# Kernel optimization log

Hardware: AMD Instinct MI355X
Metric: run time of the kernel (lower is better)

## Reference

```python
import jax, jax.numpy as jnp
import numpy as np

B, L, HID = 4, 512, 512
H, DH = 8, 64  # num_attention_heads, attention_head_size (== rel embed size)


def setup_inputs() -> dict:
    key = jax.random.key(0)
    ks = jax.random.split(key, 9)
    s = 1.0 / np.sqrt(HID)
    return {
        "hidden_states": jax.random.normal(ks[0], (B, L, HID), jnp.float32),
        "heads": jnp.zeros((B, 1, L, L), jnp.float32),  # additive mask, 0 = valid arc
        "rels": jax.random.normal(ks[1], (B, L, L, DH), jnp.float32),
        "Wq": jax.random.normal(ks[2], (HID, HID), jnp.float32) * s,
        "bq": jnp.zeros((HID,), jnp.float32),
        "Wk": jax.random.normal(ks[3], (HID, HID), jnp.float32) * s,
        "bk": jnp.zeros((HID,), jnp.float32),
        "Wv": jax.random.normal(ks[4], (HID, HID), jnp.float32) * s,
        "bv": jnp.zeros((HID,), jnp.float32),
    }


def _heads_split(x):
    # (B, L, H*DH) -> (B, H, L, DH)
    return x.reshape(B, L, H, DH).transpose(0, 2, 1, 3)


def reference(hidden_states, heads, rels, Wq, bq, Wk, bk, Wv, bv):
    q = _heads_split(hidden_states @ Wq.T + bq)  # (B,H,L,DH)
    k = _heads_split(hidden_states @ Wk.T + bk)
    v = _heads_split(hidden_states @ Wv.T + bv)

    scores = jnp.einsum("bhqd,bhkd->bhqk", q, k)
    # relation-augmented scores: sum_d q[b,h,q,d] * rels[b,q,k,d]
    rel_scores = jnp.einsum("bhqd,bqkd->bhqk", q, rels)
    scores = (scores + rel_scores) / np.sqrt(DH) + heads  # heads broadcasts over H

    probs = jax.nn.softmax(scores, axis=-1)  # dropout is identity at eval

    ctx = jnp.einsum("bhqk,bhkd->bhqd", probs, v)
    # relation-weighted values: sum_k probs[b,h,q,k] * rels[b,q,k,d]
    ctx = ctx + jnp.einsum("bhqk,bqkd->bhqd", probs, rels)

    return ctx.transpose(0, 2, 1, 3).reshape(B, L, H * DH)
```

## Files before the change

### kernel.cpp

```cpp
#include <hip/hip_runtime.h>
#include <stdint.h>


__global__ __launch_bounds__(256)
void wtrans(const float* __restrict__ Wq, const float* __restrict__ Wk,
            const float* __restrict__ Wv, float* __restrict__ WT)
{
    __shared__ float tile[64*65];
    const int z  = blockIdx.z;
    const float* W = (z==0) ? Wq : (z==1) ? Wk : Wv;
    const int kt = blockIdx.x * 64;
    const int ot = blockIdx.y * 64;
    const int t  = threadIdx.x;

    {
        const int c4 = (t & 15) * 4;
        #pragma unroll
        for (int i = 0; i < 4; i++) {
            const int r = (t >> 4) + i*16;
            const float4 v4 = *(const float4*)(W + (size_t)(ot + r)*512 + kt + c4);
            tile[r*65 + c4 + 0] = v4.x;
            tile[r*65 + c4 + 1] = v4.y;
            tile[r*65 + c4 + 2] = v4.z;
            tile[r*65 + c4 + 3] = v4.w;
        }
    }
    __syncthreads();
    {
        const int c4 = (t & 15) * 4;
        float* dst = WT + (size_t)z*262144;
        #pragma unroll
        for (int i = 0; i < 4; i++) {
            const int r2 = (t >> 4) + i*16;
            float4 v4;
            v4.x = tile[(c4+0)*65 + r2];
            v4.y = tile[(c4+1)*65 + r2];
            v4.z = tile[(c4+2)*65 + r2];
            v4.w = tile[(c4+3)*65 + r2];
            *(float4*)(dst + (size_t)(kt + r2)*512 + ot + c4) = v4;
        }
    }
}

__global__ __launch_bounds__(256)
void qkv_gemm(const float* __restrict__ X, const float* __restrict__ WT,
              const float* __restrict__ bq, const float* __restrict__ bk,
              const float* __restrict__ bv,
              float* __restrict__ qf, float* __restrict__ kTb, float* __restrict__ vf)
{
    __shared__ __align__(16) float Xs[16][512];
    const int z  = blockIdx.y;
    const int m0 = blockIdx.x * 16;
    const float* WTz = WT + (size_t)z*262144;
    const float* bb  = (z==0) ? bq : (z==1) ? bk : bv;

    const int t = threadIdx.x;
    {
        const int r = t >> 4, c0 = (t & 15) * 32;
        const float4* src = (const float4*)(X + (size_t)(m0 + r)*512 + c0);
        float4* dstl = (float4*)(&Xs[r][c0]);
        #pragma unroll
        for (int i = 0; i < 8; i++) dstl[i] = src[i];
    }
    __syncthreads();

    const int ob   = t & 127;
    const int msub = (t >> 7) * 8;
    float acc[8][4] = {};

    #pragma unroll 2
    for (int k = 0; k < 512; k += 4) {
        float w[4][4];
        #pragma unroll
        for (int kk = 0; kk < 4; kk++)
            #pragma unroll
            for (int j = 0; j < 4; j++)
                w[kk][j] = WTz[(size_t)(k+kk)*512 + ob + 128*j];
        #pragma unroll
        for (int mm = 0; mm < 8; mm++) {
            const float4 x4 = *(const float4*)(&Xs[msub + mm][k]);
            #pragma unroll
            for (int j = 0; j < 4; j++) {
                acc[mm][j] = fmaf(x4.x, w[0][j], acc[mm][j]);
                acc[mm][j] = fmaf(x4.y, w[1][j], acc[mm][j]);
                acc[mm][j] = fmaf(x4.z, w[2][j], acc[mm][j]);
                acc[mm][j] = fmaf(x4.w, w[3][j], acc[mm][j]);
            }
        }
    }

    const int b     = m0 >> 9;
    const int lbase = (m0 & 511) + msub;
    #pragma unroll
    for (int j = 0; j < 4; j++) {
        const int o = ob + 128*j;
        const float bo = bb[o];
        const int h = o >> 6, d = o & 63;
        if (z == 1) {
            float* dst = kTb + ((size_t)(b*8 + h)*64 + d)*512 + lbase;
            *(float4*)(dst + 0) = make_float4(acc[0][j]+bo, acc[1][j]+bo,
                                              acc[2][j]+bo, acc[3][j]+bo);
            *(float4*)(dst + 4) = make_float4(acc[4][j]+bo, acc[5][j]+bo,
                                              acc[6][j]+bo, acc[7][j]+bo);
        } else {
            float* dst = ((z==0) ? qf : vf) + ((size_t)(b*8 + h)*512 + lbase)*64 + d;
            #pragma unroll
            for (int mm = 0; mm < 8; mm++) dst[(size_t)mm*64] = acc[mm][j] + bo;
        }
    }
}

__global__ __launch_bounds__(512)
void attn_flash(const float* __restrict__ qf, const float* __restrict__ kT,
                const float* __restrict__ vf, const float* __restrict__ rels,
                const float* __restrict__ heads, float* __restrict__ out)
{
    __shared__ __align__(16) float rl[4*64*64];

    const int bid = blockIdx.x;
    const int wg  = (bid & 7) * 64 + (bid >> 3);
    const int b   = wg >> 7;
    const int q0  = (wg & 127) * 4;

    const int t = threadIdx.x, h = t >> 6, lane = t & 63;

    const float* kTh = kT + ((size_t)(b*8 + h)*64)*512;
    const float* vfh = vf + ((size_t)(b*8 + h)*512)*64;
    const float* qh  = qf + ((size_t)(b*8 + h)*512 + q0)*64;

    float ctx[4] = {0.f, 0.f, 0.f, 0.f};
    float m[4]   = {-3.0e38f, -3.0e38f, -3.0e38f, -3.0e38f};
    float s[4]   = {0.f, 0.f, 0.f, 0.f};

    const int sqi = t >> 7;
    const int su  = t & 127;
    const int sk  = su >> 1;
    const int sdh = (su & 1) * 32;
    const int sc4 = sdh >> 2;
    const int skx = sk & 15;
    const float* srcq = rels + ((size_t)(b*512 + q0 + sqi))*512*64;
    float* wb = rl + sqi*4096 + sk*64;

    for (int kt = 0; kt < 8; kt++) {
        __syncthreads();
        {
            const float* src = srcq + ((size_t)(kt*64 + sk))*64 + sdh;
            #pragma unroll
            for (int i = 0; i < 8; i++) {
                const float4 v4 = *(const float4*)(src + 4*i);
                *(float4*)(wb + 4*((sc4 + i) ^ skx)) = v4;
            }
        }
        __syncthreads();

        const int kg = kt*64 + lane;
        const int kx4 = lane & 15;
        const float* rr = rl + lane*64;
        float sc[4] = {0.f, 0.f, 0.f, 0.f};
        #pragma unroll 4
        for (int d0 = 0; d0 < 64; d0 += 4) {
            const float k0 = kTh[(size_t)(d0+0)*512 + kg];
            const float k1 = kTh[(size_t)(d0+1)*512 + kg];
            const float k2 = kTh[(size_t)(d0+2)*512 + kg];
            const float k3 = kTh[(size_t)(d0+3)*512 + kg];
            #pragma unroll
            for (int qi = 0; qi < 4; qi++) {
                const float4 q4 = *(const float4*)(qh + (size_t)qi*64 + d0);
                const float4 r4 = *(const float4*)(rr + qi*4096
                                                   + 4*((d0 >> 2) ^ kx4));
                float a = sc[qi];
                a = fmaf(q4.x, k0, a);  a = fmaf(q4.x, r4.x, a);
                a = fmaf(q4.y, k1, a);  a = fmaf(q4.y, r4.y, a);
                a = fmaf(q4.z, k2, a);  a = fmaf(q4.z, r4.z, a);
                a = fmaf(q4.w, k3, a);  a = fmaf(q4.w, r4.w, a);
                sc[qi] = a;
            }
        }

        float P[4];
        #pragma unroll
        for (int qi = 0; qi < 4; qi++) {
            float S = sc[qi]*0.125f
                    + heads[((size_t)(b*512 + q0 + qi))*512 + kg];
            float mt = S;
            #pragma unroll
            for (int w = 1; w < 64; w <<= 1) mt = fmaxf(mt, __shfl_xor(mt, w));
            const float mn = fmaxf(m[qi], mt);
            const float al = __expf(m[qi] - mn);
            const float p  = __expf(S - mn);
            float ps = p;
            #pragma unroll
            for (int w = 1; w < 64; w <<= 1) ps += __shfl_xor(ps, w);
            s[qi]   = s[qi]*al + ps;
            ctx[qi] = ctx[qi]*al;
            m[qi]   = mn;
            P[qi]   = p;
        }

        const float* vtile = vfh + (size_t)(kt*64)*64 + lane;
        const int l3 = lane & 3, lc = lane >> 2;
        #pragma unroll 8
        for (int kk = 0; kk < 64; kk++) {
            const float v = vtile[(size_t)kk*64];
            const float* rb = rl + kk*64 + (l3 | ((lc ^ (kk & 15)) << 2));
            #pragma unroll
            for (int qi = 0; qi < 4; qi++) {
                const float pk = __int_as_float(
                    __builtin_amdgcn_readlane(__float_as_int(P[qi]), kk));
                ctx[qi] = fmaf(pk, v + rb[qi*4096], ctx[qi]);
            }
        }
    }

    #pragma unroll
    for (int qi = 0; qi < 4; qi++)
        out[((size_t)(b*512 + q0 + qi))*512 + h*64 + lane] = ctx[qi] / s[qi];
}

extern "C" void kernel_launch(void* const* d_in, const int* in_sizes, int n_in,
                              void* d_out, int out_size, void* d_ws, size_t ws_size,
                              hipStream_t stream)
{
    (void)in_sizes; (void)n_in; (void)out_size; (void)ws_size;

    const float* hidden = (const float*)d_in[0];
    const float* heads  = (const float*)d_in[1];
    const float* rels   = (const float*)d_in[2];
    const float* Wq = (const float*)d_in[3];
    const float* bq = (const float*)d_in[4];
    const float* Wk = (const float*)d_in[5];
    const float* bk = (const float*)d_in[6];
    const float* Wv = (const float*)d_in[7];
    const float* bv = (const float*)d_in[8];
    float* outF = (float*)d_out;

    float* ws = (float*)d_ws;
    float* qf  = ws;
    float* kTb = ws + 1048576;
    float* vf  = ws + 2097152;

    float* WT = outF;

    wtrans<<<dim3(8, 8, 3), 256, 0, stream>>>(Wq, Wk, Wv, WT);
    qkv_gemm<<<dim3(128, 3), 256, 0, stream>>>(hidden, WT, bq, bk, bv, qf, kTb, vf);
    attn_flash<<<dim3(512), 512, 0, stream>>>(qf, kTb, vf, rels, heads, outF);
}
```

Before: 581.1 us.

## Register-prefetch rels tiles, vectorize PV loop and retile QKV GEMM

The attention kernel now loads the next rels tile into registers while computing on the current tile held in shared memory, so global latency overlaps compute. The P·(V+R) loop is remapped so each lane owns one query and four head dims, using float4 loads of V and rels instead of scalar loads per query. The QKV GEMM uses 8-row tiles with float4 weight loads and float4 output stores, and launches twice as many blocks. The trade-off is more register pressure from the staging buffer, plus select logic to pick per-lane softmax values.

```diff
diff --git a/kernel.cpp b/kernel.cpp
--- a/kernel.cpp
+++ b/kernel.cpp
@@ -48,64 +48,62 @@
               const float* __restrict__ bv,
               float* __restrict__ qf, float* __restrict__ kTb, float* __restrict__ vf)
 {
-    __shared__ __align__(16) float Xs[16][512];
+    __shared__ __align__(16) float Xs[8][512];
     const int z  = blockIdx.y;
-    const int m0 = blockIdx.x * 16;
+    const int m0 = blockIdx.x * 8;
     const float* WTz = WT + (size_t)z*262144;
     const float* bb  = (z==0) ? bq : (z==1) ? bk : bv;
 
     const int t = threadIdx.x;
     {
-        const int r = t >> 4, c0 = (t & 15) * 32;
+        const int r = t >> 5, c0 = (t & 31) * 16;
         const float4* src = (const float4*)(X + (size_t)(m0 + r)*512 + c0);
-        float4* dstl = (float4*)(&Xs[r][c0]);
-        #pragma unroll
-        for (int i = 0; i < 8; i++) dstl[i] = src[i];
+        float4* d4 = (float4*)(&Xs[r][c0]);
+        d4[0]=src[0]; d4[1]=src[1]; d4[2]=src[2]; d4[3]=src[3];
     }
     __syncthreads();
 
-    const int ob   = t & 127;
-    const int msub = (t >> 7) * 8;
-    float acc[8][4] = {};
+    const int o0 = (t & 127) * 4;
+    const int mh = (t >> 7) * 4;
+    float acc[4][4] = {};
 
     #pragma unroll 2
     for (int k = 0; k < 512; k += 4) {
-        float w[4][4];
+        float4 w4[4];
         #pragma unroll
         for (int kk = 0; kk < 4; kk++)
-            #pragma unroll
-            for (int j = 0; j < 4; j++)
-                w[kk][j] = WTz[(size_t)(k+kk)*512 + ob + 128*j];
-        #pragma unroll
-        for (int mm = 0; mm < 8; mm++) {
-            const float4 x4 = *(const float4*)(&Xs[msub + mm][k]);
+            w4[kk] = *(const float4*)(WTz + (size_t)(k+kk)*512 + o0);
+        #pragma unroll
+        for (int mm = 0; mm < 4; mm++) {
+            const float4 x4 = *(const float4*)(&Xs[mh + mm][k]);
             #pragma unroll
             for (int j = 0; j < 4; j++) {
-                acc[mm][j] = fmaf(x4.x, w[0][j], acc[mm][j]);
-                acc[mm][j] = fmaf(x4.y, w[1][j], acc[mm][j]);
-                acc[mm][j] = fmaf(x4.z, w[2][j], acc[mm][j]);
-                acc[mm][j] = fmaf(x4.w, w[3][j], acc[mm][j]);
+                acc[mm][j] = fmaf(x4.x, ((const float*)&w4[0])[j], acc[mm][j]);
+                acc[mm][j] = fmaf(x4.y, ((const float*)&w4[1])[j], acc[mm][j]);
+                acc[mm][j] = fmaf(x4.z, ((const float*)&w4[2])[j], acc[mm][j]);
+                acc[mm][j] = fmaf(x4.w, ((const float*)&w4[3])[j], acc[mm][j]);
             }
         }
     }
 
-    const int b     = m0 >> 9;
-    const int lbase = (m0 & 511) + msub;
-    #pragma unroll
-    for (int j = 0; j < 4; j++) {
-        const int o = ob + 128*j;
-        const float bo = bb[o];
-        const int h = o >> 6, d = o & 63;
-        if (z == 1) {
-            float* dst = kTb + ((size_t)(b*8 + h)*64 + d)*512 + lbase;
-            *(float4*)(dst + 0) = make_float4(acc[0][j]+bo, acc[1][j]+bo,
-                                              acc[2][j]+bo, acc[3][j]+bo);
-            *(float4*)(dst + 4) = make_float4(acc[4][j]+bo, acc[5][j]+bo,
-                                              acc[6][j]+bo, acc[7][j]+bo);
-        } else {
-            float* dst = ((z==0) ? qf : vf) + ((size_t)(b*8 + h)*512 + lbase)*64 + d;
-            #pragma unroll
-            for (int mm = 0; mm < 8; mm++) dst[(size_t)mm*64] = acc[mm][j] + bo;
+    const float4 b4 = *(const float4*)(bb + o0);
+    const int b = m0 >> 9, lbase = (m0 & 511) + mh;
+    const int h = o0 >> 6, d0 = o0 & 63;
+    if (z == 1) {
+        #pragma unroll
+        for (int j = 0; j < 4; j++) {
+            const float bj = ((const float*)&b4)[j];
+            const float4 vv = make_float4(acc[0][j]+bj, acc[1][j]+bj,
+                                          acc[2][j]+bj, acc[3][j]+bj);
+            *(float4*)(kTb + ((size_t)(b*8 + h)*64 + d0 + j)*512 + lbase) = vv;
+        }
+    } else {
+        float* dst = (z==0) ? qf : vf;
+        #pragma unroll
+        for (int mm = 0; mm < 4; mm++) {
+            const float4 vv = make_float4(acc[mm][0]+b4.x, acc[mm][1]+b4.y,
+                                          acc[mm][2]+b4.z, acc[mm][3]+b4.w);
+            *(float4*)(dst + ((size_t)(b*8 + h)*512 + lbase + mm)*64 + d0) = vv;
         }
     }
 }
@@ -128,7 +126,11 @@
     const float* vfh = vf + ((size_t)(b*8 + h)*512)*64;
     const float* qh  = qf + ((size_t)(b*8 + h)*512 + q0)*64;
 
-    float ctx[4] = {0.f, 0.f, 0.f, 0.f};
+    const int qp = lane >> 4;
+    const int dq = lane & 15;
+    const float* vq = vfh + 4*dq;
+
+    float ctx4[4] = {0.f, 0.f, 0.f, 0.f};
     float m[4]   = {-3.0e38f, -3.0e38f, -3.0e38f, -3.0e38f};
     float s[4]   = {0.f, 0.f, 0.f, 0.f};
 
@@ -138,20 +140,25 @@
     const int sdh = (su & 1) * 32;
     const int sc4 = sdh >> 2;
     const int skx = sk & 15;
-    const float* srcq = rels + ((size_t)(b*512 + q0 + sqi))*512*64;
+    const float* srcq = rels + ((size_t)(b*512 + q0 + sqi))*512*64
+                             + (size_t)sk*64 + sdh;
     float* wb = rl + sqi*4096 + sk*64;
+
+    float4 stg[8];
+    #pragma unroll
+    for (int i = 0; i < 8; i++) stg[i] = *(const float4*)(srcq + 4*i);
 
     for (int kt = 0; kt < 8; kt++) {
         __syncthreads();
-        {
-            const float* src = srcq + ((size_t)(kt*64 + sk))*64 + sdh;
-            #pragma unroll
-            for (int i = 0; i < 8; i++) {
-                const float4 v4 = *(const float4*)(src + 4*i);
-                *(float4*)(wb + 4*((sc4 + i) ^ skx)) = v4;
-            }
-        }
+        #pragma unroll
+        for (int i = 0; i < 8; i++)
+            *(float4*)(wb + 4*((sc4 + i) ^ skx)) = stg[i];
         __syncthreads();
+        if (kt < 7) {
+            const float* nsrc = srcq + (size_t)(kt+1)*64*64;
+            #pragma unroll
+            for (int i = 0; i < 8; i++) stg[i] = *(const float4*)(nsrc + 4*i);
+        }
 
         const int kg = kt*64 + lane;
         const int kx4 = lane & 15;
@@ -177,7 +184,7 @@
             }
         }
 
-        float P[4];
+        float P[4], al[4];
         #pragma unroll
         for (int qi = 0; qi < 4; qi++) {
             float S = sc[qi]*0.125f
@@ -186,35 +193,45 @@
             #pragma unroll
             for (int w = 1; w < 64; w <<= 1) mt = fmaxf(mt, __shfl_xor(mt, w));
             const float mn = fmaxf(m[qi], mt);
-            const float al = __expf(m[qi] - mn);
+            al[qi] = __expf(m[qi] - mn);
             const float p  = __expf(S - mn);
             float ps = p;
             #pragma unroll
             for (int w = 1; w < 64; w <<= 1) ps += __shfl_xor(ps, w);
-            s[qi]   = s[qi]*al + ps;
-            ctx[qi] = ctx[qi]*al;
-            m[qi]   = mn;
-            P[qi]   = p;
-        }
-
-        const float* vtile = vfh + (size_t)(kt*64)*64 + lane;
-        const int l3 = lane & 3, lc = lane >> 2;
+            s[qi] = s[qi]*al[qi] + ps;
+            m[qi] = mn;
+            P[qi] = p;
+        }
+        const float alsel = (qp==0) ? al[0] : (qp==1) ? al[1]
+                          : (qp==2) ? al[2] : al[3];
+        ctx4[0] *= alsel; ctx4[1] *= alsel; ctx4[2] *= alsel; ctx4[3] *= alsel;
+
+        const float* vt = vq + (size_t)(kt*64)*64;
+        const float* rbase = rl + qp*4096;
         #pragma unroll 8
         for (int kk = 0; kk < 64; kk++) {
-            const float v = vtile[(size_t)kk*64];
-            const float* rb = rl + kk*64 + (l3 | ((lc ^ (kk & 15)) << 2));
-            #pragma unroll
-            for (int qi = 0; qi < 4; qi++) {
-                const float pk = __int_as_float(
-                    __builtin_amdgcn_readlane(__float_as_int(P[qi]), kk));
-                ctx[qi] = fmaf(pk, v + rb[qi*4096], ctx[qi]);
-            }
-        }
-    }
-
-    #pragma unroll
-    for (int qi = 0; qi < 4; qi++)
-        out[((size_t)(b*512 + q0 + qi))*512 + h*64 + lane] = ctx[qi] / s[qi];
+            const float4 v4 = *(const float4*)(vt + (size_t)kk*64);
+            const float4 r4 = *(const float4*)(rbase + kk*64 + 4*(dq ^ (kk & 15)));
+            const float p0 = __int_as_float(
+                __builtin_amdgcn_readlane(__float_as_int(P[0]), kk));
+            const float p1 = __int_as_float(
+                __builtin_amdgcn_readlane(__float_as_int(P[1]), kk));
+            const float p2 = __int_as_float(
+                __builtin_amdgcn_readlane(__float_as_int(P[2]), kk));
+            const float p3 = __int_as_float(
+                __builtin_amdgcn_readlane(__float_as_int(P[3]), kk));
+            const float pk = (qp==0) ? p0 : (qp==1) ? p1 : (qp==2) ? p2 : p3;
+            ctx4[0] = fmaf(pk, v4.x + r4.x, ctx4[0]);
+            ctx4[1] = fmaf(pk, v4.y + r4.y, ctx4[1]);
+            ctx4[2] = fmaf(pk, v4.z + r4.z, ctx4[2]);
+            ctx4[3] = fmaf(pk, v4.w + r4.w, ctx4[3]);
+        }
+    }
+
+    const float ssel = (qp==0) ? s[0] : (qp==1) ? s[1] : (qp==2) ? s[2] : s[3];
+    const float inv = 1.f / ssel;
+    const float4 o4 = make_float4(ctx4[0]*inv, ctx4[1]*inv, ctx4[2]*inv, ctx4[3]*inv);
+    *(float4*)(out + ((size_t)(b*512 + q0 + qp))*512 + h*64 + 4*dq) = o4;
 }
 
 extern "C" void kernel_launch(void* const* d_in, const int* in_sizes, int n_in,
@@ -242,6 +259,6 @@
     float* WT = outF;
 
     wtrans<<<dim3(8, 8, 3), 256, 0, stream>>>(Wq, Wk, Wv, WT);
-    qkv_gemm<<<dim3(128, 3), 256, 0, stream>>>(hidden, WT, bq, bk, bv, qf, kTb, vf);
+    qkv_gemm<<<dim3(256, 3), 256, 0, stream>>>(hidden, WT, bq, bk, bv, qf, kTb, vf);
     attn_flash<<<dim3(512), 512, 0, stream>>>(qf, kTb, vf, rels, heads, outF);
 }
```

New measurement: 720.5 us. +24.0%, slower.
